# Kernel tuning notes

Measured on AMD Instinct MI355X. Metric: run time of the kernel, lower is better.

## Reference

```python
import jax, jax.numpy as jnp
import numpy as np

R = 16      # num_rels
NB = 16     # num_bases
N2 = 8192   # dp2 neighbours (layer-0 sampled nodes)
N1 = 1024   # dp1 neighbours (layer-1 sampled nodes)
NOUT = 256  # output batch nodes
F = 128     # feat_size
E = 64      # embed_size
C = 32      # num_classes


def setup_inputs() -> dict:
    key = jax.random.key(0)
    ks = jax.random.split(key, 8)
    g = lambda k, sh, scale: jax.random.normal(k, sh, dtype=jnp.float32) * scale
    return {
        "X_batch": g(ks[0], (N2, F), 1.0),
        "sel_idx": jnp.arange(N2, dtype=jnp.int64) if jax.config.jax_enable_x64 else jnp.arange(N2, dtype=jnp.int32),
        "A0": g(ks[1], (N1, R * N2), 1.0 / np.sqrt(R * N2)),
        "A1": g(ks[2], (NOUT, R * N1), 1.0 / np.sqrt(R * N1)),
        "comp1": g(ks[3], (R, NB), 1.0 / np.sqrt(NB)),
        "bases1": g(ks[4], (NB, F, E), 1.0 / np.sqrt(F)),
        "comp2": g(ks[5], (R, NB), 1.0 / np.sqrt(NB)),
        "bases2": g(ks[6], (NB, E, C), 1.0 / np.sqrt(E)),
        "bias1": jnp.zeros((E,), jnp.float32),
        "bias2": jnp.zeros((C,), jnp.float32),
    }


def reference(X_batch, sel_idx, A0, A1, comp1, bases1, comp2, bases2, bias1, bias2):
    # gather the rows of X_batch corresponding to dp2 neighbours
    x = X_batch[sel_idx]                                  # [N2, F]
    # layer 1: basis-composed relation weights, relation-stacked matmul
    w1 = jnp.einsum('rb,beh->reh', comp1, bases1)         # [R, F, E]
    xw = jnp.einsum('ne,reh->rnh', x, w1)                 # [R, N2, E]
    h1 = A0 @ xw.reshape(R * N2, E)                       # [N1, E]
    h1 = jax.nn.relu(h1 + bias1)
    # layer 2
    w2 = jnp.einsum('rb,bho->rho', comp2, bases2)         # [R, E, C]
    h2 = jnp.einsum('nh,rhc->rnc', h1, w2)                # [R, N1, C]
    out = A1 @ h2.reshape(R * N1, C) + bias2              # [NOUT, C]
    return out
```

## Files before the change

kernel.cpp:

```cpp
#include <hip/hip_runtime.h>

#define RR_ 16
#define N2_ 8192
#define N1_ 1024
#define NOUT_ 256
#define F_ 128
#define E_ 64
#define C_ 32
#define KBIG_ 131072

typedef __attribute__((ext_vector_type(4))) float f32x4;
typedef __attribute__((ext_vector_type(8))) short short8;

#define MFMA(a,b,c) __builtin_amdgcn_mfma_f32_16x16x32_bf16((a),(b),(c),0,0,0)

__device__ __forceinline__ unsigned short f2bf(float f) {
  unsigned int u = __builtin_bit_cast(unsigned int, f);
  u += 0x7fffu + ((u >> 16) & 1u);
  return (unsigned short)(u >> 16);
}

__device__ __forceinline__ short8 cvt8(f32x4 v0, f32x4 v1) {
  short8 r;
  r[0] = (short)f2bf(v0[0]); r[1] = (short)f2bf(v0[1]);
  r[2] = (short)f2bf(v0[2]); r[3] = (short)f2bf(v0[3]);
  r[4] = (short)f2bf(v1[0]); r[5] = (short)f2bf(v1[1]);
  r[6] = (short)f2bf(v1[2]); r[7] = (short)f2bf(v1[3]);
  return r;
}

__global__ __launch_bounds__(256) void k_prep(
    const float* __restrict__ comp1, const float* __restrict__ bases1,
    const float* __restrict__ comp2, const float* __restrict__ bases2,
    const float* __restrict__ bias2,
    short* __restrict__ w1T, short* __restrict__ w2T,
    float* __restrict__ h1f, float* __restrict__ out)
{
  int bid = blockIdx.x, t = threadIdx.x;
  if (bid < 32) {
    int base = bid * 4096;
    for (int i = 0; i < 16; ++i) {
      int e = base + i * 256 + t;
      int r = e >> 13, rem = e & 8191;
      int h = rem >> 7, f = rem & 127;
      float s = 0.f;
      #pragma unroll
      for (int b = 0; b < 16; ++b) s += comp1[r * 16 + b] * bases1[b * 8192 + f * 64 + h];
      w1T[e] = (short)f2bf(s);
    }
  } else if (bid < 40) {
    int base = (bid - 32) * 4096;
    for (int i = 0; i < 16; ++i) {
      int e = base + i * 256 + t;
      int r = e >> 11, rem = e & 2047;
      int c = rem >> 6, h = rem & 63;
      float s = 0.f;
      #pragma unroll
      for (int b = 0; b < 16; ++b) s += comp2[r * 16 + b] * bases2[b * 2048 + h * 32 + c];
      w2T[e] = (short)f2bf(s);
    }
  } else if (bid < 48) {
    int base = (bid - 40) * 8192;
    f32x4 z = {0.f, 0.f, 0.f, 0.f};
    for (int i = 0; i < 8; ++i)
      *(f32x4*)(h1f + base + i * 1024 + t * 4) = z;
  } else {
    for (int i = 0; i < 32; ++i) {
      int e = i * 256 + t;
      out[e] = bias2[e & 31];
    }
  }
}

__global__ __launch_bounds__(256) void k_xw(
    const float* __restrict__ X, const int* __restrict__ sel,
    const short* __restrict__ w1T, short* __restrict__ xwT)
{
  int w = blockIdx.x * 4 + (threadIdx.x >> 6);
  int lane = threadIdx.x & 63, lr = lane & 15, lg = lane >> 4;
  int r = w >> 8;
  int n0 = (w & 255) * 32;

  bool is64 = (sel[1] == 0 && sel[2] == 1);
  int i0 = is64 ? sel[2 * (n0 + lr)] : sel[n0 + lr];
  int i1 = is64 ? sel[2 * (n0 + 16 + lr)] : sel[n0 + 16 + lr];

  const short* aBase = w1T + r * 8192 + lr * 128 + 8 * lg;
  const float* b0p = X + (size_t)i0 * 128 + 8 * lg;
  const float* b1p = X + (size_t)i1 * 128 + 8 * lg;

  f32x4 acc[4][2] = {};
  #pragma unroll
  for (int ks = 0; ks < 4; ++ks) {
    short8 a[4];
    #pragma unroll
    for (int mf = 0; mf < 4; ++mf)
      a[mf] = *(const short8*)(aBase + mf * 2048 + ks * 32);
    short8 b[2];
    b[0] = cvt8(*(const f32x4*)(b0p + ks * 32), *(const f32x4*)(b0p + ks * 32 + 4));
    b[1] = cvt8(*(const f32x4*)(b1p + ks * 32), *(const f32x4*)(b1p + ks * 32 + 4));
    #pragma unroll
    for (int mf = 0; mf < 4; ++mf)
      #pragma unroll
      for (int nf = 0; nf < 2; ++nf)
        acc[mf][nf] = MFMA(a[mf], b[nf], acc[mf][nf]);
  }
  #pragma unroll
  for (int mf = 0; mf < 4; ++mf)
    #pragma unroll
    for (int nf = 0; nf < 2; ++nf)
      #pragma unroll
      for (int rr = 0; rr < 4; ++rr) {
        int h = mf * 16 + 4 * lg + rr;
        int col = r * 8192 + n0 + nf * 16 + lr;
        xwT[(size_t)h * KBIG_ + col] = (short)f2bf(acc[mf][nf][rr]);
      }
}

__global__ __launch_bounds__(256) void k_h1(
    const float* __restrict__ A0, const short* __restrict__ xwT,
    float* __restrict__ h1f)
{
  int w = blockIdx.x * 4 + (threadIdx.x >> 6);
  int lane = threadIdx.x & 63, lr = lane & 15, lg = lane >> 4;
  int mt = w >> 7;
  int ch = w & 127;
  int m0 = mt * 64;
  size_t kc = (size_t)ch * 1024;

  const float* aBase = A0 + (size_t)(m0 + lr) * KBIG_ + kc + 8 * lg;
  const short* bBase = xwT + (size_t)lr * KBIG_ + kc + 8 * lg;

  f32x4 acc[4][4] = {};
  for (int ks = 0; ks < 32; ++ks) {
    short8 a[4];
    #pragma unroll
    for (int mf = 0; mf < 4; ++mf) {
      const float* p = aBase + (size_t)mf * 16 * KBIG_ + ks * 32;
      f32x4 v0 = __builtin_nontemporal_load((const f32x4*)p);
      f32x4 v1 = __builtin_nontemporal_load((const f32x4*)p + 1);
      a[mf] = cvt8(v0, v1);
    }
    short8 b[4];
    #pragma unroll
    for (int nf = 0; nf < 4; ++nf)
      b[nf] = *(const short8*)(bBase + (size_t)nf * 16 * KBIG_ + ks * 32);
    #pragma unroll
    for (int mf = 0; mf < 4; ++mf)
      #pragma unroll
      for (int nf = 0; nf < 4; ++nf)
        acc[mf][nf] = MFMA(a[mf], b[nf], acc[mf][nf]);
  }
  #pragma unroll
  for (int mf = 0; mf < 4; ++mf)
    #pragma unroll
    for (int nf = 0; nf < 4; ++nf)
      #pragma unroll
      for (int rr = 0; rr < 4; ++rr)
        atomicAdd(h1f + (m0 + mf * 16 + 4 * lg + rr) * 64 + nf * 16 + lr,
                  acc[mf][nf][rr]);
}

__global__ __launch_bounds__(256) void k_relu(
    const float* __restrict__ h1f, const float* __restrict__ bias1,
    short* __restrict__ h1b)
{
  int idx = (blockIdx.x * 256 + threadIdx.x) * 8;
  f32x4 v0 = *(const f32x4*)(h1f + idx);
  f32x4 v1 = *(const f32x4*)(h1f + idx + 4);
  int h = idx & 63;
  short8 o;
  #pragma unroll
  for (int j = 0; j < 4; ++j) {
    float x = v0[j] + bias1[h + j];     x = x > 0.f ? x : 0.f; o[j] = (short)f2bf(x);
  }
  #pragma unroll
  for (int j = 0; j < 4; ++j) {
    float x = v1[j] + bias1[h + 4 + j]; x = x > 0.f ? x : 0.f; o[4 + j] = (short)f2bf(x);
  }
  *(short8*)(h1b + idx) = o;
}

__global__ __launch_bounds__(256) void k_h2(
    const short* __restrict__ w2T, const short* __restrict__ h1b,
    short* __restrict__ H2T)
{
  int w = blockIdx.x * 4 + (threadIdx.x >> 6);
  int lane = threadIdx.x & 63, lr = lane & 15, lg = lane >> 4;
  int r = w >> 4;
  int n0 = (w & 15) * 64;

  f32x4 acc[2][4] = {};
  #pragma unroll
  for (int ks = 0; ks < 2; ++ks) {
    short8 a[2];
    #pragma unroll
    for (int mf = 0; mf < 2; ++mf)
      a[mf] = *(const short8*)(w2T + r * 2048 + (mf * 16 + lr) * 64 + ks * 32 + 8 * lg);
    short8 b[4];
    #pragma unroll
    for (int nf = 0; nf < 4; ++nf)
      b[nf] = *(const short8*)(h1b + (size_t)(n0 + nf * 16 + lr) * 64 + ks * 32 + 8 * lg);
    #pragma unroll
    for (int mf = 0; mf < 2; ++mf)
      #pragma unroll
      for (int nf = 0; nf < 4; ++nf)
        acc[mf][nf] = MFMA(a[mf], b[nf], acc[mf][nf]);
  }
  #pragma unroll
  for (int mf = 0; mf < 2; ++mf)
    #pragma unroll
    for (int nf = 0; nf < 4; ++nf)
      #pragma unroll
      for (int rr = 0; rr < 4; ++rr) {
        int c = mf * 16 + 4 * lg + rr;
        int col = r * 1024 + n0 + nf * 16 + lr;
        H2T[(size_t)c * 16384 + col] = (short)f2bf(acc[mf][nf][rr]);
      }
}

__global__ __launch_bounds__(256) void k_out(
    const float* __restrict__ A1, const short* __restrict__ H2T,
    float* __restrict__ out)
{
  int w = blockIdx.x * 4 + (threadIdx.x >> 6);
  int lane = threadIdx.x & 63, lr = lane & 15, lg = lane >> 4;
  int mt = w >> 7;
  int ch = w & 127;
  int m0 = mt * 64;
  size_t kc = (size_t)ch * 128;

  const float* aBase = A1 + (size_t)(m0 + lr) * 16384 + kc + 8 * lg;
  const short* bBase = H2T + (size_t)lr * 16384 + kc + 8 * lg;

  f32x4 acc[4][2] = {};
  #pragma unroll
  for (int ks = 0; ks < 4; ++ks) {
    short8 a[4];
    #pragma unroll
    for (int mf = 0; mf < 4; ++mf) {
      const float* p = aBase + (size_t)mf * 16 * 16384 + ks * 32;
      f32x4 v0 = __builtin_nontemporal_load((const f32x4*)p);
      f32x4 v1 = __builtin_nontemporal_load((const f32x4*)p + 1);
      a[mf] = cvt8(v0, v1);
    }
    short8 b[2];
    #pragma unroll
    for (int nf = 0; nf < 2; ++nf)
      b[nf] = *(const short8*)(bBase + (size_t)nf * 16 * 16384 + ks * 32);
    #pragma unroll
    for (int mf = 0; mf < 4; ++mf)
      #pragma unroll
      for (int nf = 0; nf < 2; ++nf)
        acc[mf][nf] = MFMA(a[mf], b[nf], acc[mf][nf]);
  }
  #pragma unroll
  for (int mf = 0; mf < 4; ++mf)
    #pragma unroll
    for (int nf = 0; nf < 2; ++nf)
      #pragma unroll
      for (int rr = 0; rr < 4; ++rr)
        atomicAdd(out + (m0 + mf * 16 + 4 * lg + rr) * 32 + nf * 16 + lr,
                  acc[mf][nf][rr]);
}

extern "C" void kernel_launch(void* const* d_in, const int* in_sizes, int n_in,
                              void* d_out, int out_size, void* d_ws, size_t ws_size,
                              hipStream_t stream) {
  (void)in_sizes; (void)n_in; (void)out_size; (void)ws_size;
  const float* X      = (const float*)d_in[0];
  const int*   sel    = (const int*)  d_in[1];
  const float* A0     = (const float*)d_in[2];
  const float* A1     = (const float*)d_in[3];
  const float* comp1  = (const float*)d_in[4];
  const float* bases1 = (const float*)d_in[5];
  const float* comp2  = (const float*)d_in[6];
  const float* bases2 = (const float*)d_in[7];
  const float* bias1  = (const float*)d_in[8];
  const float* bias2  = (const float*)d_in[9];
  float* out = (float*)d_out;

  char* ws = (char*)d_ws;
  short* w1T = (short*)(ws);
  short* w2T = (short*)(ws + 262144);
  short* xwT = (short*)(ws + 327680);
  float* h1f = (float*)(ws + 17104896);
  short* h1b = (short*)(ws + 17367040);
  short* H2T = (short*)(ws + 17498112);

  k_prep<<<49,   256, 0, stream>>>(comp1, bases1, comp2, bases2, bias2, w1T, w2T, h1f, out);
  k_xw  <<<1024, 256, 0, stream>>>(X, sel, w1T, xwT);
  k_h1  <<<512,  256, 0, stream>>>(A0, xwT, h1f);
  k_relu<<<32,   256, 0, stream>>>(h1f, bias1, h1b);
  k_h2  <<<64,   256, 0, stream>>>(w2T, h1b, H2T);
  k_out <<<128,  256, 0, stream>>>(A1, H2T, out);
}
```

Before: 241.0 us.

## Replace split-K atomic accumulation with partial buffers and reduction kernels

The two split-K matmuls (A0·xw and A1·H2) now write per-chunk partial tiles to workspace instead of doing float atomicAdds into shared outputs. New reduction kernels sum the 128 partials and apply bias/ReLU, and the zero-init work in the prep kernel is removed. This targets atomic contention on the small outputs, but adds a 32 MB partial buffer write and read for h1 plus an extra kernel launch.

```diff
diff --git a/kernel.cpp b/kernel.cpp
--- a/kernel.cpp
+++ b/kernel.cpp
@@ -11,6 +11,7 @@
 
 typedef __attribute__((ext_vector_type(4))) float f32x4;
 typedef __attribute__((ext_vector_type(8))) short short8;
+typedef __attribute__((ext_vector_type(4))) short s16x4;
 
 #define MFMA(a,b,c) __builtin_amdgcn_mfma_f32_16x16x32_bf16((a),(b),(c),0,0,0)
 
@@ -32,9 +33,7 @@
 __global__ __launch_bounds__(256) void k_prep(
     const float* __restrict__ comp1, const float* __restrict__ bases1,
     const float* __restrict__ comp2, const float* __restrict__ bases2,
-    const float* __restrict__ bias2,
-    short* __restrict__ w1T, short* __restrict__ w2T,
-    float* __restrict__ h1f, float* __restrict__ out)
+    short* __restrict__ w1T, short* __restrict__ w2T)
 {
   int bid = blockIdx.x, t = threadIdx.x;
   if (bid < 32) {
@@ -48,7 +47,7 @@
       for (int b = 0; b < 16; ++b) s += comp1[r * 16 + b] * bases1[b * 8192 + f * 64 + h];
       w1T[e] = (short)f2bf(s);
     }
-  } else if (bid < 40) {
+  } else {
     int base = (bid - 32) * 4096;
     for (int i = 0; i < 16; ++i) {
       int e = base + i * 256 + t;
@@ -59,16 +58,6 @@
       for (int b = 0; b < 16; ++b) s += comp2[r * 16 + b] * bases2[b * 2048 + h * 32 + c];
       w2T[e] = (short)f2bf(s);
     }
-  } else if (bid < 48) {
-    int base = (bid - 40) * 8192;
-    f32x4 z = {0.f, 0.f, 0.f, 0.f};
-    for (int i = 0; i < 8; ++i)
-      *(f32x4*)(h1f + base + i * 1024 + t * 4) = z;
-  } else {
-    for (int i = 0; i < 32; ++i) {
-      int e = i * 256 + t;
-      out[e] = bias2[e & 31];
-    }
   }
 }
 
@@ -119,7 +108,7 @@
 
 __global__ __launch_bounds__(256) void k_h1(
     const float* __restrict__ A0, const short* __restrict__ xwT,
-    float* __restrict__ h1f)
+    float* __restrict__ h1p)
 {
   int w = blockIdx.x * 4 + (threadIdx.x >> 6);
   int lane = threadIdx.x & 63, lr = lane & 15, lg = lane >> 4;
@@ -151,34 +140,36 @@
       for (int nf = 0; nf < 4; ++nf)
         acc[mf][nf] = MFMA(a[mf], b[nf], acc[mf][nf]);
   }
+  float* base = h1p + (size_t)ch * 65536;
   #pragma unroll
   for (int mf = 0; mf < 4; ++mf)
     #pragma unroll
     for (int nf = 0; nf < 4; ++nf)
       #pragma unroll
       for (int rr = 0; rr < 4; ++rr)
-        atomicAdd(h1f + (m0 + mf * 16 + 4 * lg + rr) * 64 + nf * 16 + lr,
-                  acc[mf][nf][rr]);
-}
-
-__global__ __launch_bounds__(256) void k_relu(
-    const float* __restrict__ h1f, const float* __restrict__ bias1,
+        base[(m0 + mf * 16 + 4 * lg + rr) * 64 + nf * 16 + lr] = acc[mf][nf][rr];
+}
+
+__global__ __launch_bounds__(256) void k_red(
+    const float* __restrict__ h1p, const float* __restrict__ bias1,
     short* __restrict__ h1b)
 {
-  int idx = (blockIdx.x * 256 + threadIdx.x) * 8;
-  f32x4 v0 = *(const f32x4*)(h1f + idx);
-  f32x4 v1 = *(const f32x4*)(h1f + idx + 4);
-  int h = idx & 63;
-  short8 o;
+  int e = (blockIdx.x * 256 + threadIdx.x) * 4;
+  f32x4 s = {0.f, 0.f, 0.f, 0.f};
+  #pragma unroll 8
+  for (int c = 0; c < 128; ++c) {
+    f32x4 v = *(const f32x4*)(h1p + (size_t)c * 65536 + e);
+    s += v;
+  }
+  int h = e & 63;
+  s16x4 o;
   #pragma unroll
   for (int j = 0; j < 4; ++j) {
-    float x = v0[j] + bias1[h + j];     x = x > 0.f ? x : 0.f; o[j] = (short)f2bf(x);
-  }
-  #pragma unroll
-  for (int j = 0; j < 4; ++j) {
-    float x = v1[j] + bias1[h + 4 + j]; x = x > 0.f ? x : 0.f; o[4 + j] = (short)f2bf(x);
-  }
-  *(short8*)(h1b + idx) = o;
+    float x = s[j] + bias1[h + j];
+    x = x > 0.f ? x : 0.f;
+    o[j] = (short)f2bf(x);
+  }
+  *(s16x4*)(h1b + e) = o;
 }
 
 __global__ __launch_bounds__(256) void k_h2(
@@ -221,7 +212,7 @@
 
 __global__ __launch_bounds__(256) void k_out(
     const float* __restrict__ A1, const short* __restrict__ H2T,
-    float* __restrict__ out)
+    float* __restrict__ outp)
 {
   int w = blockIdx.x * 4 + (threadIdx.x >> 6);
   int lane = threadIdx.x & 63, lr = lane & 15, lg = lane >> 4;
@@ -254,14 +245,33 @@
       for (int nf = 0; nf < 2; ++nf)
         acc[mf][nf] = MFMA(a[mf], b[nf], acc[mf][nf]);
   }
+  float* base = outp + (size_t)ch * 8192;
   #pragma unroll
   for (int mf = 0; mf < 4; ++mf)
     #pragma unroll
     for (int nf = 0; nf < 2; ++nf)
       #pragma unroll
       for (int rr = 0; rr < 4; ++rr)
-        atomicAdd(out + (m0 + mf * 16 + 4 * lg + rr) * 32 + nf * 16 + lr,
-                  acc[mf][nf][rr]);
+        base[(m0 + mf * 16 + 4 * lg + rr) * 32 + nf * 16 + lr] = acc[mf][nf][rr];
+}
+
+__global__ __launch_bounds__(256) void k_outred(
+    const float* __restrict__ outp, const float* __restrict__ bias2,
+    float* __restrict__ out)
+{
+  int e = (blockIdx.x * 256 + threadIdx.x) * 4;
+  f32x4 s = {0.f, 0.f, 0.f, 0.f};
+  #pragma unroll 8
+  for (int c = 0; c < 128; ++c) {
+    f32x4 v = *(const f32x4*)(outp + (size_t)c * 8192 + e);
+    s += v;
+  }
+  int cc = e & 31;
+  f32x4 o;
+  #pragma unroll
+  for (int j = 0; j < 4; ++j)
+    o[j] = s[j] + bias2[cc + j];
+  *(f32x4*)(out + e) = o;
 }
 
 extern "C" void kernel_launch(void* const* d_in, const int* in_sizes, int n_in,
@@ -284,14 +294,16 @@
   short* w1T = (short*)(ws);
   short* w2T = (short*)(ws + 262144);
   short* xwT = (short*)(ws + 327680);
-  float* h1f = (float*)(ws + 17104896);
-  short* h1b = (short*)(ws + 17367040);
-  short* H2T = (short*)(ws + 17498112);
-
-  k_prep<<<49,   256, 0, stream>>>(comp1, bases1, comp2, bases2, bias2, w1T, w2T, h1f, out);
-  k_xw  <<<1024, 256, 0, stream>>>(X, sel, w1T, xwT);
-  k_h1  <<<512,  256, 0, stream>>>(A0, xwT, h1f);
-  k_relu<<<32,   256, 0, stream>>>(h1f, bias1, h1b);
-  k_h2  <<<64,   256, 0, stream>>>(w2T, h1b, H2T);
-  k_out <<<128,  256, 0, stream>>>(A1, H2T, out);
-}
+  float* h1p = (float*)(ws + 17104896);
+  short* h1b = (short*)(ws + 50659328);
+  short* H2T = (short*)(ws + 50790400);
+  float* outp= (float*)(ws + 51838976);
+
+  k_prep  <<<40,   256, 0, stream>>>(comp1, bases1, comp2, bases2, w1T, w2T);
+  k_xw    <<<1024, 256, 0, stream>>>(X, sel, w1T, xwT);
+  k_h1    <<<512,  256, 0, stream>>>(A0, xwT, h1p);
+  k_red   <<<64,   256, 0, stream>>>(h1p, bias1, h1b);
+  k_h2    <<<64,   256, 0, stream>>>(w2T, h1b, H2T);
+  k_out   <<<128,  256, 0, stream>>>(A1, H2T, outp);
+  k_outred<<<8,    256, 0, stream>>>(outp, bias2, out);
+}
```

Result: slower. 254.4 us (+5.5%).
